# Performance work log

Hardware: AMD Instinct MI355X
Metric: run time of the kernel (lower is better)

The kernel has to match this reference:

```python
import jax, jax.numpy as jnp
import numpy as np
from jax import lax

# ---- config (matches init_kwargs) ----
B, S = 8, 256
WIDTH, LEVELS, STATE, PARAM = 32, 3, 1, 1
WSIZE = (64, 64)
PAD = 1  # padding//2 with padding=2

# ---- db6 filters (pywt ordering) ----
L = 12
DEC_LO = np.array([-0.00107730108499558, 0.004777257511010651, 0.0005538422009938016,
                   -0.031582039318031156, 0.02752286553001629, 0.09750160558707936,
                   -0.12976686756709563, -0.22626469396516913, 0.3152503517092432,
                   0.7511339080215775, 0.4946238903983854, 0.11154074335008017],
                  dtype=np.float32)
REC_LO = DEC_LO[::-1].copy()
REC_HI = ((-1.0) ** np.arange(L)).astype(np.float32) * DEC_LO
DEC_HI = REC_HI[::-1].copy()
# correlation kernels: analysis = flipped dec filters (= rec), synthesis = flipped rec (= dec)
KA = jnp.asarray(np.stack([REC_LO, REC_HI]))   # [2, L]
KS = jnp.asarray(np.stack([DEC_LO, DEC_HI]))   # [2, L]


def dwt1d(x, axis):
    """Single-level analysis along axis (2 or 3) of NCHW x; symmetric pad + stride-2 conv.
    Matches pytorch_wavelets afb1d (symmetric mode, even N)."""
    b, c = x.shape[0], x.shape[1]
    pads = [(0, 0)] * 4
    pads[axis] = (L - 2, L - 2)
    xp = jnp.pad(x, pads, mode='symmetric')
    xr = xp.reshape((b * c, 1) + xp.shape[2:])
    if axis == 2:
        k = KA.reshape(2, 1, L, 1); strides = (2, 1)
    else:
        k = KA.reshape(2, 1, 1, L); strides = (1, 2)
    y = lax.conv_general_dilated(xr, k, strides, 'VALID')  # [b*c, 2, H', W']
    y = y.reshape((b, c, 2) + y.shape[2:])
    return y[:, :, 0], y[:, :, 1]


def idwt1d(lo, hi, axis):
    """Single-level synthesis along axis: zero-upsample (lhs_dilation=2) + conv, crop L-2.
    Matches pytorch_wavelets sfb1d (conv_transpose stride 2, padding L-2)."""
    b, c = lo.shape[0], lo.shape[1]
    x = jnp.stack([lo, hi], axis=2).reshape((b * c, 2) + lo.shape[2:])
    if axis == 2:
        k = KS.reshape(1, 2, L, 1); ld = (2, 1); pad = ((1, 1), (0, 0))
    else:
        k = KS.reshape(1, 2, 1, L); ld = (1, 2); pad = ((0, 0), (1, 1))
    y = lax.conv_general_dilated(x, k, (1, 1), pad, lhs_dilation=ld)  # len = 2N-L+2
    return y.reshape((b, c) + y.shape[2:])


def afb2d(x):
    xl, xh = dwt1d(x, 3)
    ll, lh = dwt1d(xl, 2)
    hl, hh = dwt1d(xh, 2)
    return ll, jnp.stack([lh, hl, hh], axis=2)  # [B,C,3,H',W']


def sfb2d(ll, yh):
    lh, hl, hh = yh[:, :, 0], yh[:, :, 1], yh[:, :, 2]
    xl = idwt1d(ll, lh, 2)
    xh = idwt1d(hl, hh, 2)
    return idwt1d(xl, xh, 3)


def interp_bilinear(w, Ho, Wo):
    """F.interpolate(mode='bilinear', align_corners=False) on [I,O,h,w]."""
    h, wd = w.shape[2], w.shape[3]
    if (h, wd) == (Ho, Wo):
        return w
    def coords(n_out, n_in):
        scale = n_in / n_out
        s = jnp.maximum((jnp.arange(n_out, dtype=jnp.float32) + 0.5) * scale - 0.5, 0.0)
        i0 = jnp.minimum(jnp.floor(s).astype(jnp.int32), n_in - 1)
        i1 = jnp.minimum(i0 + 1, n_in - 1)
        t = jnp.clip(s - i0.astype(jnp.float32), 0.0, 1.0)
        return i0, i1, t
    y0, y1, ty = coords(Ho, h)
    x0, x1, tx = coords(Wo, wd)
    wr = w[:, :, y0, :] * (1.0 - ty)[None, None, :, None] + w[:, :, y1, :] * ty[None, None, :, None]
    return wr[:, :, :, x0] * (1.0 - tx) + wr[:, :, :, x1] * tx


def wavelet_conv(x, w):
    """WaveletConv2d.forward: J-level DWT, per-subband channel mix, IDWT."""
    orig = x.shape
    ll, highs = x, []
    for _ in range(LEVELS):
        ll, yh = afb2d(ll)
        highs.append(yh)
    wi = interp_bilinear(w, ll.shape[-2], ll.shape[-1])
    out = jnp.einsum('bixy,ioxy->boxy', ll, wi)
    out_h = []
    for h in highs:
        # torch code interpolates weights to input.shape[-3:-1] == (3, Hj) and broadcasts over W
        whi = interp_bilinear(w, h.shape[-3], h.shape[-2])
        out_h.append(jnp.einsum('bixyz,ioxy->boxyz', h, whi))
    for h in reversed(out_h):
        out = out[:, :, :h.shape[-2], :h.shape[-1]]
        out = sfb2d(out, h)
    return out[:, :, :orig[2], :orig[3]]


def wno2d(u, par, x, y, fc0_w, fc0_b, wc_w, pw_w, pw_b, fc1_w, fc1_b, fc2_w, fc2_b):
    b, s0, s1 = u.shape[0], u.shape[1], u.shape[2]
    gridx = jnp.broadcast_to(x[:, :, None, None], (b, s0, s1, 1))
    gridy = jnp.broadcast_to(y[:, None, :, None], (b, s0, s1, 1))
    h = jnp.concatenate([u, par, gridx, gridy], axis=-1)      # [B,S0,S1,4]
    h = h @ fc0_w.T + fc0_b                                   # [B,S0,S1,width]
    h = jnp.transpose(h, (0, 3, 1, 2))                        # NCHW
    h = jnp.pad(h, ((0, 0), (0, 0), (PAD, PAD), (PAD, PAD)), mode='reflect')
    for i in range(4):
        u1 = wavelet_conv(h, wc_w[i])
        u2 = jnp.einsum('bixy,oi->boxy', h, pw_w[i]) + pw_b[i][None, :, None, None]
        h = u1 + u2
        if i < 3:
            h = jax.nn.gelu(h, approximate=False)
    h = h[:, :, PAD:-PAD, PAD:-PAD]
    h = jnp.transpose(h, (0, 2, 3, 1))
    h = jax.nn.gelu(h @ fc1_w.T + fc1_b, approximate=False)
    return h @ fc2_w.T + fc2_b                                # [B,S0,S1,state]


def setup_inputs() -> dict:
    key = jax.random.key(0)
    ks = jax.random.split(key, 16)
    f32 = jnp.float32
    scale = 1.0 / (WIDTH * WIDTH)
    return {
        'u': jax.random.normal(ks[0], (B, S, S, STATE), f32),
        'par': jax.random.normal(ks[1], (B, S, S, PARAM), f32),
        'x': jax.random.uniform(ks[2], (B, S), f32),
        'y': jax.random.uniform(ks[3], (B, S), f32),
        'fc0_w': 0.3 * jax.random.normal(ks[4], (WIDTH, STATE + PARAM + 2), f32),
        'fc0_b': jnp.zeros((WIDTH,), f32),
        'wc_w': scale * jax.random.uniform(ks[5], (4, WIDTH, WIDTH) + WSIZE, f32),
        'pw_w': (1.0 / np.sqrt(WIDTH)) * jax.random.normal(ks[6], (4, WIDTH, WIDTH), f32),
        'pw_b': jnp.zeros((4, WIDTH), f32),
        'fc1_w': (1.0 / np.sqrt(WIDTH)) * jax.random.normal(ks[7], (128, WIDTH), f32),
        'fc1_b': jnp.zeros((128,), f32),
        'fc2_w': (1.0 / np.sqrt(128.0)) * jax.random.normal(ks[8], (STATE, 128), f32),
        'fc2_b': jnp.zeros((STATE,), f32),
    }


def reference(u, par, x, y, fc0_w, fc0_b, wc_w, pw_w, pw_b, fc1_w, fc1_b, fc2_w, fc2_b):
    return wno2d(u, par, x, y, fc0_w, fc0_b, wc_w, pw_w, pw_b, fc1_w, fc1_b, fc2_w, fc2_b)
```

## Files before the change

kernel.cpp:

```cpp
#include <hip/hip_runtime.h>
#include <math.h>

#define W0f  (-0.00107730108499558f)
#define W1f  (0.004777257511010651f)
#define W2f  (0.0005538422009938016f)
#define W3f  (-0.031582039318031156f)
#define W4f  (0.02752286553001629f)
#define W5f  (0.09750160558707936f)
#define W6f  (-0.12976686756709563f)
#define W7f  (-0.22626469396516913f)
#define W8f  (0.3152503517092432f)
#define W9f  (0.7511339080215775f)
#define W10f (0.4946238903983854f)
#define W11f (0.11154074335008017f)

__constant__ float cKA0[12] = {W11f,W10f,W9f,W8f,W7f,W6f,W5f,W4f,W3f,W2f,W1f,W0f};
__constant__ float cKA1[12] = {W0f,-W1f,W2f,-W3f,W4f,-W5f,W6f,-W7f,W8f,-W9f,W10f,-W11f};
__constant__ float cKS0[12] = {W0f,W1f,W2f,W3f,W4f,W5f,W6f,W7f,W8f,W9f,W10f,W11f};
__constant__ float cKS1[12] = {-W11f,W10f,-W9f,W8f,-W7f,W6f,-W5f,W4f,-W3f,W2f,-W1f,W0f};

#define S1c 134
#define S2c 72
#define S3c 41
#define A3c 1681
#define N1c 4596736UL
#define N2c 1327104UL
#define N3c 430336UL

__device__ __forceinline__ float gelu_f(float x) {
    float z  = x * 0.70710678118654752440f;
    float az = fabsf(z);
    float t  = __builtin_amdgcn_rcpf(1.0f + 0.3275911f * az);
    float p  = t * (0.254829592f + t * (-0.284496736f + t * (1.421413741f +
               t * (-1.453152027f + t * 1.061405429f))));
    float e  = __expf(-az * az);
    float er = copysignf(1.0f - p * e, z);
    return 0.5f * x * (1.0f + er);
}

__global__ __launch_bounds__(256) void dwt2d(
    const float* __restrict__ in, float* __restrict__ ll, float* __restrict__ lh,
    float* __restrict__ hl, float* __restrict__ hh, int H, int W, int Ho, int Wo) {
    int c   = blockIdx.z;
    int ty0 = blockIdx.y * 16;
    int tx0 = blockIdx.x * 16;
    const float* img = in + (size_t)c * H * W;
    __shared__ float sIn[42][44];
    __shared__ float rlo[42][17];
    __shared__ float rhi[42][17];
    int tid = threadIdx.x;
    for (int idx = tid; idx < 42 * 42; idx += 256) {
        int r = idx / 42, q = idx % 42;
        int gy = 2 * ty0 - 10 + r;
        int gx = 2 * tx0 - 10 + q;
        gy = gy < 0 ? -1 - gy : (gy >= H ? 2 * H - 1 - gy : gy);
        gx = gx < 0 ? -1 - gx : (gx >= W ? 2 * W - 1 - gx : gx);
        sIn[r][q] = img[gy * W + gx];
    }
    __syncthreads();
    for (int idx = tid; idx < 42 * 16; idx += 256) {
        int r = idx / 16, j = idx % 16;
        float alo = 0.f, ahi = 0.f;
        #pragma unroll
        for (int t = 0; t < 12; t++) {
            float v = sIn[r][2 * j + t];
            alo += v * cKA0[t];
            ahi += v * cKA1[t];
        }
        rlo[r][j] = alo; rhi[r][j] = ahi;
    }
    __syncthreads();
    int jy = tid / 16, jx = tid % 16;
    int oy = ty0 + jy, ox = tx0 + jx;
    if (oy < Ho && ox < Wo) {
        float a0 = 0.f, a1 = 0.f, a2 = 0.f, a3 = 0.f;
        #pragma unroll
        for (int t = 0; t < 12; t++) {
            float vl = rlo[2 * jy + t][jx];
            float vh = rhi[2 * jy + t][jx];
            a0 += vl * cKA0[t]; a1 += vl * cKA1[t];
            a2 += vh * cKA0[t]; a3 += vh * cKA1[t];
        }
        size_t o = (size_t)c * Ho * Wo + (size_t)oy * Wo + ox;
        ll[o] = a0; lh[o] = a1; hl[o] = a2; hh[o] = a3;
    }
}

__global__ __launch_bounds__(256) void dwt2d_fc0(
    const float* __restrict__ u, const float* __restrict__ par,
    const float* __restrict__ xg, const float* __restrict__ yg,
    const float* __restrict__ fw, const float* __restrict__ fb,
    float* __restrict__ ll, float* __restrict__ lh,
    float* __restrict__ hl, float* __restrict__ hh) {
    const int Hd = 258, S = 256, Ho = S1c, Wo = S1c;
    int c   = blockIdx.z;
    int b   = c >> 5, o = c & 31;
    float w0 = fw[o*4], w1 = fw[o*4+1], w2 = fw[o*4+2], w3 = fw[o*4+3], bv = fb[o];
    int ty0 = blockIdx.y * 16;
    int tx0 = blockIdx.x * 16;
    __shared__ float sIn[42][44];
    __shared__ float rlo[42][17];
    __shared__ float rhi[42][17];
    int tid = threadIdx.x;
    for (int idx = tid; idx < 42 * 42; idx += 256) {
        int r = idx / 42, q = idx % 42;
        int gy = 2 * ty0 - 10 + r;
        int gx = 2 * tx0 - 10 + q;
        gy = gy < 0 ? -1 - gy : (gy >= Hd ? 2 * Hd - 1 - gy : gy);
        gx = gx < 0 ? -1 - gx : (gx >= Hd ? 2 * Hd - 1 - gx : gx);
        int iy = gy - 1; iy = iy < 0 ? -iy : (iy >= S ? 2 * S - 2 - iy : iy);
        int ix = gx - 1; ix = ix < 0 ? -ix : (ix >= S ? 2 * S - 2 - ix : ix);
        float vu = u  [(b * S + iy) * S + ix];
        float vp = par[(b * S + iy) * S + ix];
        sIn[r][q] = w0 * vu + w1 * vp + w2 * xg[b * S + iy] + w3 * yg[b * S + ix] + bv;
    }
    __syncthreads();
    for (int idx = tid; idx < 42 * 16; idx += 256) {
        int r = idx / 16, j = idx % 16;
        float alo = 0.f, ahi = 0.f;
        #pragma unroll
        for (int t = 0; t < 12; t++) {
            float v = sIn[r][2 * j + t];
            alo += v * cKA0[t];
            ahi += v * cKA1[t];
        }
        rlo[r][j] = alo; rhi[r][j] = ahi;
    }
    __syncthreads();
    int jy = tid / 16, jx = tid % 16;
    int oy = ty0 + jy, ox = tx0 + jx;
    if (oy < Ho && ox < Wo) {
        float a0 = 0.f, a1 = 0.f, a2 = 0.f, a3 = 0.f;
        #pragma unroll
        for (int t = 0; t < 12; t++) {
            float vl = rlo[2 * jy + t][jx];
            float vh = rhi[2 * jy + t][jx];
            a0 += vl * cKA0[t]; a1 += vl * cKA1[t];
            a2 += vh * cKA0[t]; a3 += vh * cKA1[t];
        }
        size_t oo = (size_t)c * Ho * Wo + (size_t)oy * Wo + ox;
        ll[oo] = a0; lh[oo] = a1; hl[oo] = a2; hh[oo] = a3;
    }
}

__global__ __launch_bounds__(256) void idwt2d(
    const float* __restrict__ ll, const float* __restrict__ lh,
    const float* __restrict__ hl, const float* __restrict__ hh,
    float* __restrict__ out, const float* __restrict__ pb,
    int h, int w, int Oh, int Ow, int do_gelu) {
    int c   = blockIdx.z;
    int my0 = blockIdx.y * 16;
    int nx0 = blockIdx.x * 16;
    __shared__ float sll[21][22], slh[21][22], shl[21][22], shh[21][22];
    __shared__ float sxl[32][22], sxh[32][22];
    int tid = threadIdx.x;
    size_t cb = (size_t)c * h * w;
    float bias = pb ? pb[c & 31] : 0.f;
    for (int idx = tid; idx < 21 * 21; idx += 256) {
        int r = idx / 21, q = idx % 21;
        int gy = min(my0 + r, h - 1);
        int gx = min(nx0 + q, w - 1);
        size_t g = cb + (size_t)gy * w + gx;
        sll[r][q] = ll[g]; slh[r][q] = lh[g];
        shl[r][q] = hl[g]; shh[r][q] = hh[g];
    }
    __syncthreads();
    for (int idx = tid; idx < 32 * 21; idx += 256) {
        int r = idx / 21, q = idx % 21;
        int mp = r >> 1, p = r & 1;
        float al = 0.f, ah = 0.f;
        #pragma unroll
        for (int s = 0; s < 6; s++) {
            float k0 = cKS0[2 * s + 1 - p];
            float k1 = cKS1[2 * s + 1 - p];
            al += sll[mp + s][q] * k0 + slh[mp + s][q] * k1;
            ah += shl[mp + s][q] * k0 + shh[mp + s][q] * k1;
        }
        sxl[r][q] = al; sxh[r][q] = ah;
    }
    __syncthreads();
    for (int idx = tid; idx < 32 * 32; idx += 256) {
        int r = idx / 32, q2 = idx % 32;
        int np = q2 >> 1, q = q2 & 1;
        int oy = 2 * my0 + r, ox = 2 * nx0 + q2;
        if (oy < Oh && ox < Ow) {
            float a = bias;
            #pragma unroll
            for (int s = 0; s < 6; s++) {
                float k0 = cKS0[2 * s + 1 - q];
                float k1 = cKS1[2 * s + 1 - q];
                a += sxl[r][np + s] * k0 + sxh[r][np + s] * k1;
            }
            if (do_gelu) a = gelu_f(a);
            out[(size_t)c * Oh * Ow + (size_t)oy * Ow + ox] = a;
        }
    }
}

__global__ __launch_bounds__(256) void transpose_all(
    const float* __restrict__ w, float* __restrict__ wT) {
    __shared__ float t[64][65];
    int l  = blockIdx.y >> 4;
    int by = (blockIdx.y & 15) * 64;
    int bx = blockIdx.x * 64;
    const float* wl = w  + (size_t)l * 4194304;
    float* wTl      = wT + (size_t)l * 4194304;
    int tid = threadIdx.x;
    for (int idx = tid; idx < 4096; idx += 256) {
        int r = idx >> 6, q = idx & 63;
        t[r][q] = wl[(size_t)(by + r) * 4096 + bx + q];
    }
    __syncthreads();
    for (int idx = tid; idx < 4096; idx += 256) {
        int r = idx >> 6, q = idx & 63;
        wTl[(size_t)(bx + r) * 1024 + by + q] = t[q][r];
    }
}

#define PLc 2480128UL
__global__ __launch_bounds__(256) void interp4(
    const float* __restrict__ wT, const float* __restrict__ pw,
    float* __restrict__ wout) {
    int l = blockIdx.y;
    const float* wTl = wT + (size_t)l * 4194304;
    const float* pwl = pw + (size_t)l * 1024;
    float* base = wout + (size_t)l * PLc;
    __shared__ float spw[1024];
    int tid = threadIdx.x;
    for (int k = tid; k < 1024; k += 256) spw[k] = pwl[(k & 31) * 32 + (k >> 5)];
    __syncthreads();
    int bId = blockIdx.x;
    float* dst; int Ho, Wo, p;
    if (bId < A3c)                          { dst = base;                                 Ho = S3c; Wo = S3c; p = bId; }
    else if (bId < A3c + 3 * S1c)           { dst = base + A3c * 1024;                    Ho = 3;   Wo = S1c; p = bId - A3c; }
    else if (bId < A3c + 3 * (S1c + S2c))   { dst = base + (A3c + 3 * S1c) * 1024;        Ho = 3;   Wo = S2c; p = bId - A3c - 3 * S1c; }
    else                                    { dst = base + (A3c + 3 * (S1c + S2c)) * 1024; Ho = 3;  Wo = S3c; p = bId - A3c - 3 * (S1c + S2c); }
    int y = p / Wo, x = p % Wo;
    float sy = fmaxf((y + 0.5f) * (64.0f / Ho) - 0.5f, 0.0f);
    int y0 = min((int)sy, 63), y1 = min(y0 + 1, 63);
    float ty = fminf(sy - (float)y0, 1.0f);
    float sx = fmaxf((x + 0.5f) * (64.0f / Wo) - 0.5f, 0.0f);
    int x0 = min((int)sx, 63), x1 = min(x0 + 1, 63);
    float tx = fminf(sx - (float)x0, 1.0f);
    float c00 = (1.f - ty) * (1.f - tx), c01 = (1.f - ty) * tx;
    float c10 = ty * (1.f - tx),         c11 = ty * tx;
    const float4* s00 = (const float4*)(wTl + (size_t)(y0 * 64 + x0) * 1024);
    const float4* s01 = (const float4*)(wTl + (size_t)(y0 * 64 + x1) * 1024);
    const float4* s10 = (const float4*)(wTl + (size_t)(y1 * 64 + x0) * 1024);
    const float4* s11 = (const float4*)(wTl + (size_t)(y1 * 64 + x1) * 1024);
    float4* op = (float4*)(dst + (size_t)p * 1024);
    int k = tid;
    float4 a = s00[k], b = s01[k], c = s10[k], d = s11[k];
    float4 pw4 = *(const float4*)&spw[k * 4];
    float4 r;
    r.x = c00*a.x + c01*b.x + c10*c.x + c11*d.x + pw4.x;
    r.y = c00*a.y + c01*b.y + c10*c.y + c11*d.y + pw4.y;
    r.z = c00*a.z + c01*b.z + c10*c.z + c11*d.z + pw4.z;
    r.w = c00*a.w + c01*b.w + c10*c.w + c11*d.w + pw4.w;
    op[k] = r;
}

__global__ __launch_bounds__(256) void mix_all(
    float* __restrict__ ll3, float* __restrict__ lh3,
    float* __restrict__ lh2, float* __restrict__ lh1,
    const float* __restrict__ wl) {
    const float* wll = wl;
    const float* wh1 = wl + A3c * 1024;
    const float* wh2 = wh1 + 3 * S1c * 1024;
    const float* wh3 = wh2 + 3 * S2c * 1024;
    __shared__ float sw[1024];
    __shared__ float sv[256];
    int tid = threadIdx.x;
    int bid = blockIdx.x;
    if (bid < A3c) {
        const float* wb = wll + (size_t)bid * 1024;
        for (int k = tid; k < 1024; k += 256) sw[k] = wb[k];
        int b = tid >> 5, i = tid & 31;
        sv[tid] = ll3[((size_t)(b * 32 + i)) * A3c + bid];
        __syncthreads();
        float acc = 0.f;
        #pragma unroll
        for (int k = 0; k < 32; k++) acc += sv[b * 32 + k] * sw[k * 32 + i];
        ll3[((size_t)(b * 32 + i)) * A3c + bid] = acc;
        return;
    }
    int t = bid - A3c;
    float* hb; const float* wb; int Hs, Ws, s, y, xb; size_t bstride;
    if (t < 2 * S3c * 3) {
        Hs = Ws = S3c; bstride = N3c;
        int per = 2 * S3c; s = t / per; int r = t % per; y = r / 2; xb = r % 2;
        hb = lh3; wb = wh3;
    } else if ((t -= 2 * S3c * 3) < 3 * S2c * 3) {
        Hs = Ws = S2c; bstride = N2c;
        int per = 3 * S2c; s = t / per; int r = t % per; y = r / 3; xb = r % 3;
        hb = lh2; wb = wh2;
    } else {
        t -= 3 * S2c * 3;
        Hs = Ws = S1c; bstride = N1c;
        int per = 5 * S1c; s = t / per; int r = t % per; y = r / 5; xb = r % 5;
        hb = lh1; wb = wh1;
    }
    hb += (size_t)s * bstride;
    wb += ((size_t)s * Hs + y) * 1024;
    for (int k = tid; k < 1024; k += 256) sw[k] = wb[k];
    __syncthreads();
    int q = xb * 256 + tid;
    if (q >= 8 * Ws) return;
    int b = q / Ws, x = q % Ws;
    size_t base = ((size_t)(b * 32) * Hs + y) * Ws + x;
    size_t cs = (size_t)Hs * Ws;
    float acc[32];
    #pragma unroll
    for (int o = 0; o < 32; o++) acc[o] = 0.f;
    for (int i = 0; i < 32; i++) {
        float v = hb[base + (size_t)i * cs];
        #pragma unroll
        for (int o4 = 0; o4 < 8; o4++) {
            float4 w4 = *(const float4*)&sw[i * 32 + o4 * 4];
            acc[o4*4+0] += v * w4.x; acc[o4*4+1] += v * w4.y;
            acc[o4*4+2] += v * w4.z; acc[o4*4+3] += v * w4.w;
        }
    }
    #pragma unroll
    for (int o = 0; o < 32; o++) hb[base + (size_t)o * cs] = acc[o];
}

__global__ __launch_bounds__(256) void head_k(
    const float* __restrict__ h, const float* __restrict__ w1, const float* __restrict__ b1,
    const float* __restrict__ w2, const float* __restrict__ b2, float* __restrict__ out) {
    __shared__ float sw1[4096];
    __shared__ float sb1[128];
    __shared__ float sw2[128];
    int tid = threadIdx.x;
    for (int k = tid; k < 4096; k += 256) sw1[k] = w1[k];
    if (tid < 128) { sb1[tid] = b1[tid]; sw2[tid] = w2[tid]; }
    __syncthreads();
    const int Hp = 258;
    const int QP = 262144;
    int g0 = blockIdx.x * 256 + tid;
    float in[2][32];
    #pragma unroll
    for (int p = 0; p < 2; p++) {
        int gid = g0 + p * QP;
        int b = gid >> 16, r = gid & 65535;
        int yy = r >> 8, xx = r & 255;
        size_t base = (size_t)b * 32 * Hp * Hp + (size_t)(yy + 1) * Hp + (xx + 1);
        #pragma unroll
        for (int i = 0; i < 32; i++) in[p][i] = h[base + (size_t)i * Hp * Hp];
    }
    float acc0 = 0.f, acc1 = 0.f;
    for (int j = 0; j < 128; j++) {
        float h0 = sb1[j], h1 = h0;
        #pragma unroll
        for (int i4 = 0; i4 < 8; i4++) {
            float4 wv = *(const float4*)&sw1[j * 32 + i4 * 4];
            h0 += wv.x * in[0][i4*4+0] + wv.y * in[0][i4*4+1] + wv.z * in[0][i4*4+2] + wv.w * in[0][i4*4+3];
            h1 += wv.x * in[1][i4*4+0] + wv.y * in[1][i4*4+1] + wv.z * in[1][i4*4+2] + wv.w * in[1][i4*4+3];
        }
        float w2j = sw2[j];
        acc0 += w2j * gelu_f(h0);
        acc1 += w2j * gelu_f(h1);
    }
    float b2v = b2[0];
    out[g0     ] = acc0 + b2v;
    out[g0 + QP] = acc1 + b2v;
}

extern "C" void kernel_launch(void* const* d_in, const int* in_sizes, int n_in,
                              void* d_out, int out_size, void* d_ws, size_t ws_size,
                              hipStream_t stream) {
    (void)in_sizes; (void)n_in; (void)out_size;
    const float* u    = (const float*)d_in[0];
    const float* par  = (const float*)d_in[1];
    const float* xg   = (const float*)d_in[2];
    const float* yg   = (const float*)d_in[3];
    const float* fc0w = (const float*)d_in[4];
    const float* fc0b = (const float*)d_in[5];
    const float* wcw  = (const float*)d_in[6];
    const float* pww  = (const float*)d_in[7];
    const float* pwb  = (const float*)d_in[8];
    const float* fc1w = (const float*)d_in[9];
    const float* fc1b = (const float*)d_in[10];
    const float* fc2w = (const float*)d_in[11];
    const float* fc2b = (const float*)d_in[12];
    float* out = (float*)d_out;
    float* ws  = (float*)d_ws;

    const int Hp = 258;
    const size_t HW = (size_t)Hp * Hp;
    const size_t NH = 256 * HW;
    const int S1 = S1c, S2 = S2c, S3 = S3c;
    const size_t N1 = N1c, N2 = N2c, N3 = N3c;

    float* H   = ws;
    float* ll1 = H   + NH;
    float* lh1 = ll1 + N1;
    float* hl1 = lh1 + N1;
    float* hh1 = hl1 + N1;
    float* ll2 = hh1 + N1;
    float* lh2 = ll2 + N2;
    float* hl2 = lh2 + N2;
    float* hh2 = hl2 + N2;
    float* ll3 = hh2 + N2;
    float* lh3 = ll3 + N3;
    float* hl3 = lh3 + N3;
    float* hh3 = hl3 + N3;
    float* w4  = hh3 + N3;
    size_t needed = (size_t)(w4 + 4 * PLc - ws) * sizeof(float);
    if (ws_size < needed) return;
    float* wTall = lh1;

    transpose_all<<<dim3(64, 64), 256, 0, stream>>>(wcw, wTall);
    int nInterp = A3c + 3 * (S1 + S2 + S3);
    interp4<<<dim3(nInterp, 4), 256, 0, stream>>>(wTall, pww, w4);

    const int nMix = A3c + 2 * S3 * 3 + 3 * S2 * 3 + 5 * S1 * 3;

    for (int l = 0; l < 4; l++) {
        const float* wl = w4 + (size_t)l * PLc;

        if (l == 0) {
            dwt2d_fc0<<<dim3((S1 + 15) / 16, (S1 + 15) / 16, 256), 256, 0, stream>>>(
                u, par, xg, yg, fc0w, fc0b, ll1, lh1, hl1, hh1);
        } else {
            dwt2d<<<dim3((S1 + 15) / 16, (S1 + 15) / 16, 256), 256, 0, stream>>>(
                H, ll1, lh1, hl1, hh1, Hp, Hp, S1, S1);
        }
        dwt2d<<<dim3((S2 + 15) / 16, (S2 + 15) / 16, 256), 256, 0, stream>>>(
            ll1, ll2, lh2, hl2, hh2, S1, S1, S2, S2);
        dwt2d<<<dim3((S3 + 15) / 16, (S3 + 15) / 16, 256), 256, 0, stream>>>(
            ll2, ll3, lh3, hl3, hh3, S2, S2, S3, S3);

        mix_all<<<nMix, 256, 0, stream>>>(ll3, lh3, lh2, lh1, wl);

        idwt2d<<<dim3((S2 + 31) / 32, (S2 + 31) / 32, 256), 256, 0, stream>>>(
            ll3, lh3, hl3, hh3, ll2, nullptr, S3, S3, S2, S2, 0);
        idwt2d<<<dim3((S1 + 31) / 32, (S1 + 31) / 32, 256), 256, 0, stream>>>(
            ll2, lh2, hl2, hh2, ll1, nullptr, S2, S2, S1, S1, 0);
        idwt2d<<<dim3((Hp + 31) / 32, (Hp + 31) / 32, 256), 256, 0, stream>>>(
            ll1, lh1, hl1, hh1, H, pwb + (size_t)l * 32, S1, S1, Hp, Hp, (l < 3) ? 1 : 0);
    }

    head_k<<<(8 * 256 * 256 / 2 + 255) / 256, 256, 0, stream>>>(H, fc1w, fc1b, fc2w, fc2b, out);
}
```

Baseline: 1.183 ms.

## Fuse level-1 inverse wavelet, GELU and next layer's forward DWT into one kernel

```diff
diff --git a/kernel.cpp b/kernel.cpp
--- a/kernel.cpp
+++ b/kernel.cpp
@@ -26,6 +26,7 @@
 #define N1c 4596736UL
 #define N2c 1327104UL
 #define N3c 430336UL
+#define PLc 2480128UL
 
 __device__ __forceinline__ float gelu_f(float x) {
     float z  = x * 0.70710678118654752440f;
@@ -197,6 +198,96 @@
     }
 }
 
+__global__ __launch_bounds__(256) void idwt_dwt(
+    const float* __restrict__ ll, const float* __restrict__ lh,
+    const float* __restrict__ hl, const float* __restrict__ hh,
+    float* __restrict__ oll, float* __restrict__ olh,
+    float* __restrict__ ohl, float* __restrict__ ohh,
+    const float* __restrict__ pb) {
+    const int hb = S1c, Hd = 258, Wo = S1c;
+    int c = blockIdx.z;
+    int ty0 = blockIdx.y * 16, tx0 = blockIdx.x * 16;
+    int ay = 2 * ty0 - 10, ax = 2 * tx0 - 10;
+    float bias = pb[c & 31];
+    __shared__ float sll[27][28], slh[27][28], shl[27][28], shh[27][28];
+    __shared__ float sxl[42][28], sxh[42][28];
+    __shared__ float sIn[42][44];
+    __shared__ float rlo[42][17], rhi[42][17];
+    int tid = threadIdx.x;
+    int ylo = ay < 0 ? 0 : ay;  int yhi = ay + 41;
+    if (yhi >= Hd) { ylo = min(ylo, 2 * Hd - 1 - yhi); yhi = Hd - 1; }
+    int xlo = ax < 0 ? 0 : ax;  int xhi = ax + 41;
+    if (xhi >= Hd) { xlo = min(xlo, 2 * Hd - 1 - xhi); xhi = Hd - 1; }
+    int brow0 = ylo >> 1, bcol0 = xlo >> 1;
+    size_t cb = (size_t)c * hb * hb;
+    for (int idx = tid; idx < 27 * 27; idx += 256) {
+        int r = idx / 27, q = idx % 27;
+        int gy = min(brow0 + r, hb - 1);
+        int gx = min(bcol0 + q, hb - 1);
+        size_t g = cb + (size_t)gy * hb + gx;
+        sll[r][q] = ll[g]; slh[r][q] = lh[g];
+        shl[r][q] = hl[g]; shh[r][q] = hh[g];
+    }
+    __syncthreads();
+    for (int idx = tid; idx < 42 * 27; idx += 256) {
+        int yr = idx / 27, q = idx % 27;
+        int t = ay + yr;
+        int gy = t < 0 ? -1 - t : (t >= Hd ? 2 * Hd - 1 - t : t);
+        int m = (gy >> 1) - brow0, p = gy & 1;
+        float al = 0.f, ah = 0.f;
+        #pragma unroll
+        for (int s = 0; s < 6; s++) {
+            float k0 = cKS0[2 * s + 1 - p];
+            float k1 = cKS1[2 * s + 1 - p];
+            al += sll[m + s][q] * k0 + slh[m + s][q] * k1;
+            ah += shl[m + s][q] * k0 + shh[m + s][q] * k1;
+        }
+        sxl[yr][q] = al; sxh[yr][q] = ah;
+    }
+    __syncthreads();
+    for (int idx = tid; idx < 42 * 42; idx += 256) {
+        int yr = idx / 42, xr = idx % 42;
+        int t = ax + xr;
+        int gx = t < 0 ? -1 - t : (t >= Hd ? 2 * Hd - 1 - t : t);
+        int n = (gx >> 1) - bcol0, q = gx & 1;
+        float a = bias;
+        #pragma unroll
+        for (int s = 0; s < 6; s++) {
+            float k0 = cKS0[2 * s + 1 - q];
+            float k1 = cKS1[2 * s + 1 - q];
+            a += sxl[yr][n + s] * k0 + sxh[yr][n + s] * k1;
+        }
+        sIn[yr][xr] = gelu_f(a);
+    }
+    __syncthreads();
+    for (int idx = tid; idx < 42 * 16; idx += 256) {
+        int r = idx / 16, j = idx % 16;
+        float alo = 0.f, ahi = 0.f;
+        #pragma unroll
+        for (int t = 0; t < 12; t++) {
+            float v = sIn[r][2 * j + t];
+            alo += v * cKA0[t];
+            ahi += v * cKA1[t];
+        }
+        rlo[r][j] = alo; rhi[r][j] = ahi;
+    }
+    __syncthreads();
+    int jy = tid / 16, jx = tid % 16;
+    int oy = ty0 + jy, ox = tx0 + jx;
+    if (oy < Wo && ox < Wo) {
+        float a0 = 0.f, a1 = 0.f, a2 = 0.f, a3 = 0.f;
+        #pragma unroll
+        for (int t = 0; t < 12; t++) {
+            float vl = rlo[2 * jy + t][jx];
+            float vh = rhi[2 * jy + t][jx];
+            a0 += vl * cKA0[t]; a1 += vl * cKA1[t];
+            a2 += vh * cKA0[t]; a3 += vh * cKA1[t];
+        }
+        size_t o = cb + (size_t)oy * Wo + ox;
+        oll[o] = a0; olh[o] = a1; ohl[o] = a2; ohh[o] = a3;
+    }
+}
+
 __global__ __launch_bounds__(256) void transpose_all(
     const float* __restrict__ w, float* __restrict__ wT) {
     __shared__ float t[64][65];
@@ -217,7 +308,6 @@
     }
 }
 
-#define PLc 2480128UL
 __global__ __launch_bounds__(256) void interp4(
     const float* __restrict__ wT, const float* __restrict__ pw,
     float* __restrict__ wout) {
@@ -336,34 +426,24 @@
     if (tid < 128) { sb1[tid] = b1[tid]; sw2[tid] = w2[tid]; }
     __syncthreads();
     const int Hp = 258;
-    const int QP = 262144;
-    int g0 = blockIdx.x * 256 + tid;
-    float in[2][32];
+    int gid = blockIdx.x * 256 + tid;
+    int b = gid >> 16, r = gid & 65535;
+    int yy = r >> 8, xx = r & 255;
+    size_t base = (size_t)b * 32 * Hp * Hp + (size_t)(yy + 1) * Hp + (xx + 1);
+    float in[32];
     #pragma unroll
-    for (int p = 0; p < 2; p++) {
-        int gid = g0 + p * QP;
-        int b = gid >> 16, r = gid & 65535;
-        int yy = r >> 8, xx = r & 255;
-        size_t base = (size_t)b * 32 * Hp * Hp + (size_t)(yy + 1) * Hp + (xx + 1);
-        #pragma unroll
-        for (int i = 0; i < 32; i++) in[p][i] = h[base + (size_t)i * Hp * Hp];
-    }
-    float acc0 = 0.f, acc1 = 0.f;
+    for (int i = 0; i < 32; i++) in[i] = h[base + (size_t)i * Hp * Hp];
+    float acc = 0.f;
     for (int j = 0; j < 128; j++) {
-        float h0 = sb1[j], h1 = h0;
+        float h0 = sb1[j];
         #pragma unroll
         for (int i4 = 0; i4 < 8; i4++) {
             float4 wv = *(const float4*)&sw1[j * 32 + i4 * 4];
-            h0 += wv.x * in[0][i4*4+0] + wv.y * in[0][i4*4+1] + wv.z * in[0][i4*4+2] + wv.w * in[0][i4*4+3];
-            h1 += wv.x * in[1][i4*4+0] + wv.y * in[1][i4*4+1] + wv.z * in[1][i4*4+2] + wv.w * in[1][i4*4+3];
-        }
-        float w2j = sw2[j];
-        acc0 += w2j * gelu_f(h0);
-        acc1 += w2j * gelu_f(h1);
-    }
-    float b2v = b2[0];
-    out[g0     ] = acc0 + b2v;
-    out[g0 + QP] = acc1 + b2v;
+            h0 += wv.x * in[i4*4+0] + wv.y * in[i4*4+1] + wv.z * in[i4*4+2] + wv.w * in[i4*4+3];
+        }
+        acc += sw2[j] * gelu_f(h0);
+    }
+    out[gid] = acc + b2[0];
 }
 
 extern "C" void kernel_launch(void* const* d_in, const int* in_sizes, int n_in,
@@ -386,18 +466,12 @@
     float* out = (float*)d_out;
     float* ws  = (float*)d_ws;
 
-    const int Hp = 258;
-    const size_t HW = (size_t)Hp * Hp;
-    const size_t NH = 256 * HW;
     const int S1 = S1c, S2 = S2c, S3 = S3c;
     const size_t N1 = N1c, N2 = N2c, N3 = N3c;
 
-    float* H   = ws;
-    float* ll1 = H   + NH;
-    float* lh1 = ll1 + N1;
-    float* hl1 = lh1 + N1;
-    float* hh1 = hl1 + N1;
-    float* ll2 = hh1 + N1;
+    float* A   = ws;
+    float* Bb  = A   + 4 * N1;
+    float* ll2 = Bb  + 4 * N1;
     float* lh2 = ll2 + N2;
     float* hl2 = lh2 + N2;
     float* hh2 = hl2 + N2;
@@ -408,38 +482,46 @@
     float* w4  = hh3 + N3;
     size_t needed = (size_t)(w4 + 4 * PLc - ws) * sizeof(float);
     if (ws_size < needed) return;
-    float* wTall = lh1;
+    float* H     = A;
+    float* wTall = Bb;
 
     transpose_all<<<dim3(64, 64), 256, 0, stream>>>(wcw, wTall);
     int nInterp = A3c + 3 * (S1 + S2 + S3);
     interp4<<<dim3(nInterp, 4), 256, 0, stream>>>(wTall, pww, w4);
 
+    dwt2d_fc0<<<dim3((S1 + 15) / 16, (S1 + 15) / 16, 256), 256, 0, stream>>>(
+        u, par, xg, yg, fc0w, fc0b, A, A + N1, A + 2 * N1, A + 3 * N1);
+
     const int nMix = A3c + 2 * S3 * 3 + 3 * S2 * 3 + 5 * S1 * 3;
 
     for (int l = 0; l < 4; l++) {
+        float* inb  = (l & 1) ? Bb : A;
+        float* outb = (l & 1) ? A  : Bb;
         const float* wl = w4 + (size_t)l * PLc;
 
-        if (l == 0) {
-            dwt2d_fc0<<<dim3((S1 + 15) / 16, (S1 + 15) / 16, 256), 256, 0, stream>>>(
-                u, par, xg, yg, fc0w, fc0b, ll1, lh1, hl1, hh1);
-        } else {
-            dwt2d<<<dim3((S1 + 15) / 16, (S1 + 15) / 16, 256), 256, 0, stream>>>(
-                H, ll1, lh1, hl1, hh1, Hp, Hp, S1, S1);
-        }
         dwt2d<<<dim3((S2 + 15) / 16, (S2 + 15) / 16, 256), 256, 0, stream>>>(
-            ll1, ll2, lh2, hl2, hh2, S1, S1, S2, S2);
+            inb, ll2, lh2, hl2, hh2, S1, S1, S2, S2);
         dwt2d<<<dim3((S3 + 15) / 16, (S3 + 15) / 16, 256), 256, 0, stream>>>(
             ll2, ll3, lh3, hl3, hh3, S2, S2, S3, S3);
 
-        mix_all<<<nMix, 256, 0, stream>>>(ll3, lh3, lh2, lh1, wl);
+        mix_all<<<nMix, 256, 0, stream>>>(ll3, lh3, lh2, inb + N1, wl);
 
         idwt2d<<<dim3((S2 + 31) / 32, (S2 + 31) / 32, 256), 256, 0, stream>>>(
             ll3, lh3, hl3, hh3, ll2, nullptr, S3, S3, S2, S2, 0);
         idwt2d<<<dim3((S1 + 31) / 32, (S1 + 31) / 32, 256), 256, 0, stream>>>(
-            ll2, lh2, hl2, hh2, ll1, nullptr, S2, S2, S1, S1, 0);
-        idwt2d<<<dim3((Hp + 31) / 32, (Hp + 31) / 32, 256), 256, 0, stream>>>(
-            ll1, lh1, hl1, hh1, H, pwb + (size_t)l * 32, S1, S1, Hp, Hp, (l < 3) ? 1 : 0);
-    }
-
-    head_k<<<(8 * 256 * 256 / 2 + 255) / 256, 256, 0, stream>>>(H, fc1w, fc1b, fc2w, fc2b, out);
-}
+            ll2, lh2, hl2, hh2, inb, nullptr, S2, S2, S1, S1, 0);
+
+        if (l < 3) {
+            idwt_dwt<<<dim3((S1 + 15) / 16, (S1 + 15) / 16, 256), 256, 0, stream>>>(
+                inb, inb + N1, inb + 2 * N1, inb + 3 * N1,
+                outb, outb + N1, outb + 2 * N1, outb + 3 * N1,
+                pwb + (size_t)l * 32);
+        } else {
+            idwt2d<<<dim3((258 + 31) / 32, (258 + 31) / 32, 256), 256, 0, stream>>>(
+                inb, inb + N1, inb + 2 * N1, inb + 3 * N1, H,
+                pwb + (size_t)l * 32, S1, S1, 258, 258, 0);
+        }
+    }
+
+    head_k<<<(8 * 256 * 256 + 255) / 256, 256, 0, stream>>>(H, fc1w, fc1b, fc2w, fc2b, out);
+}
```

After: 1.361 ms. 1.15x slower.
